# Kernel optimization log

Measured on AMD Instinct MI355X. Metric: run time of the kernel, lower is better.

The kernel has to match this reference:

```python
import jax, jax.numpy as jnp
import numpy as np

# --- QTIP TCQ config (matches init_kwargs) ---
M, K = 4096, 4096          # out_features, in_features
TD_X, TD_Y = 16, 16        # tile dims
L = 16                     # trellis state bits
KV = 4                     # bits consumed per step (K=2 bits/weight * V=2)
V = 2                      # weights emitted per step
TLUT_BITS = 9              # lut index bits
T_STEPS = TD_X * TD_Y // V # 128 steps per tile
NBITS = T_STEPS * KV       # 512 bits per tile (tail-biting: exactly K bits/weight)
NWORDS = NBITS // 16       # 32 int16 words per tile
NT = (M // TD_X) * (K // TD_Y)  # 65536 tiles
BATCH, SEQ = 4, 2048


def setup_inputs() -> dict:
    key = jax.random.key(0)
    k1, k2, k3 = jax.random.split(key, 3)
    inp = jax.random.normal(k1, (BATCH, SEQ, K), dtype=jnp.float32)
    # int16 buffer modeled as int32 holding arbitrary 16-bit patterns
    trellis = jax.random.randint(k2, (NT, NWORDS), 0, 65536, dtype=jnp.int32)
    tlut = jax.random.normal(k3, (2 ** TLUT_BITS, V), dtype=jnp.float32) * 0.02
    return {"inp": inp, "trellis": trellis, "tlut": tlut}


def _decode(trellis, tlut):
    """Decode bit-packed tail-biting bitshift trellis codes into dense W [M, K]."""
    words = trellis.astype(jnp.uint32) & 0xFFFF          # uint16 bit patterns
    shifts = (15 - jnp.arange(16)).astype(jnp.uint32)    # MSB-first within word
    bits = ((words[:, :, None] >> shifts) & 1).astype(jnp.int32).reshape(NT, NBITS)
    # step t reads L-bit window starting at t*KV, wrapping around (tail-biting)
    win = (jnp.arange(T_STEPS)[:, None] * KV + jnp.arange(L)[None, :]) % NBITS  # [T, L]
    bw = bits[:, win]                                    # [NT, T, L]
    pow2 = (2 ** (L - 1 - jnp.arange(L))).astype(jnp.int32)
    state = jnp.einsum('ntl,l->nt', bw, pow2)            # L-bit state per step
    code = state & (2 ** TLUT_BITS - 1)                  # low tlut_bits index the lut
    w = tlut[code].reshape(NT, TD_X, TD_Y)               # V outputs/step, row-major tile
    # tiles are laid out row-major over (M//td_x, K//td_y)
    w = w.reshape(M // TD_X, K // TD_Y, TD_X, TD_Y).transpose(0, 2, 1, 3).reshape(M, K)
    return w


def reference(inp, trellis, tlut):
    Wd = _decode(trellis, tlut)          # [M, K]
    x = inp.reshape(-1, K)               # [bs, K]
    y = x @ Wd.T                         # [bs, M]
    return y.reshape(*inp.shape[:-1], M).astype(inp.dtype)
```

## Files before the change

### kernel.cpp

```cpp
#include <hip/hip_runtime.h>
#include <hip/hip_bf16.h>

#define AS1 __attribute__((address_space(1)))
#define AS3 __attribute__((address_space(3)))

typedef __bf16 bf16x8 __attribute__((ext_vector_type(8)));
typedef float f32x4 __attribute__((ext_vector_type(4)));

#define GLOAD_LDS16(gptr, lptr) \
  __builtin_amdgcn_global_load_lds((AS1 void*)(gptr), (AS3 void*)(lptr), 16, 0, 0)

#define M_W   4096
#define K_DIM 4096
#define M_X   8192
#define NT_T  65536
#define NKT   (K_DIM/64)

#define BAR()        __builtin_amdgcn_s_barrier()
#define WAIT_VM4()   asm volatile("s_waitcnt vmcnt(4)" ::: "memory")
#define WAIT_VM0()   asm volatile("s_waitcnt vmcnt(0)" ::: "memory")

__device__ __forceinline__ unsigned short f2bf(float f) {
  unsigned int u = __float_as_uint(f);
  unsigned int r = (u + 0x7FFFu + ((u >> 16) & 1u)) >> 16;
  return (unsigned short)r;
}

__global__ void prep_kernel(const float* __restrict__ x,
                            const int* __restrict__ trellis,
                            const float* __restrict__ tlut,
                            unsigned short* __restrict__ xb,
                            unsigned short* __restrict__ W) {
  int b = blockIdx.x;
  int tid = threadIdx.x;
  if (b % 3 == 0) {
    int idx = (b / 3) * 256 + tid;
    const float4* p = reinterpret_cast<const float4*>(x) + (size_t)idx * 2;
    float4 u = p[0];
    float4 v = p[1];
    uint4 o;
    o.x = (unsigned)f2bf(u.x) | ((unsigned)f2bf(u.y) << 16);
    o.y = (unsigned)f2bf(u.z) | ((unsigned)f2bf(u.w) << 16);
    o.z = (unsigned)f2bf(v.x) | ((unsigned)f2bf(v.y) << 16);
    o.w = (unsigned)f2bf(v.z) | ((unsigned)f2bf(v.w) << 16);
    reinterpret_cast<uint4*>(xb)[idx] = o;
  } else {
    int db = b - b / 3 - 1;
    int idx = db * 256 + tid;
    int t = idx >> 7;
    int s = idx & 127;
    const unsigned int* tr = reinterpret_cast<const unsigned int*>(trellis) + t * 32;
    int w0  = s >> 2;
    int off = (s & 3) * 4;
    unsigned int a = tr[w0] & 0xFFFFu;
    unsigned int state;
    if (off == 0) {
      state = a;
    } else {
      unsigned int bb = tr[(w0 + 1) & 31] & 0xFFFFu;
      state = ((a << off) | (bb >> (16 - off))) & 0xFFFFu;
    }
    unsigned int code = state & 0x1FFu;
    float2 v = reinterpret_cast<const float2*>(tlut)[code];
    int i = t >> 8;
    int j = t & 255;
    int flat = s * 2;
    int r = flat >> 4;
    int c = flat & 15;
    unsigned int packed = (unsigned)f2bf(v.x) | ((unsigned)f2bf(v.y) << 16);
    size_t o = (size_t)(i * 16 + r) * K_DIM + (j * 16 + c);
    *reinterpret_cast<unsigned int*>(W + o) = packed;
  }
}


template<int BUF, int MH>
__device__ __forceinline__ void lda(const char* ldsc, const int* aRow, const int* kOff,
                                    bf16x8 (&af)[4][2]) {
  const char* base = ldsc + (BUF * 2 + MH) * 16384;
  #pragma unroll
  for (int fm = 0; fm < 4; ++fm)
    #pragma unroll
    for (int kh = 0; kh < 2; ++kh)
      af[fm][kh] = *(const bf16x8*)(base + aRow[fm] + kOff[kh]);
}

template<int BUF, int NH>
__device__ __forceinline__ void ldb(const char* ldsc, const int* bRow, const int* kOff,
                                    bf16x8 (&bq)[2][2]) {
  const char* base = ldsc + 65536 + (BUF * 2 + NH) * 16384;
  #pragma unroll
  for (int fn = 0; fn < 2; ++fn)
    #pragma unroll
    for (int kh = 0; kh < 2; ++kh)
      bq[fn][kh] = *(const bf16x8*)(base + bRow[fn] + kOff[kh]);
}

template<int MH, int NH>
__device__ __forceinline__ void mm(const bf16x8 (&af)[4][2], const bf16x8 (&bq)[2][2],
                                   f32x4 (&acc)[8][4]) {
  #pragma unroll
  for (int fm = 0; fm < 4; ++fm)
    #pragma unroll
    for (int fn = 0; fn < 2; ++fn)
      #pragma unroll
      for (int kh = 0; kh < 2; ++kh)
        acc[MH * 4 + fm][NH * 2 + fn] =
            __builtin_amdgcn_mfma_f32_16x16x32_bf16(af[fm][kh], bq[fn][kh],
                                                    acc[MH * 4 + fm][NH * 2 + fn], 0, 0, 0);
}

template<int BUF, int HALF>
__device__ __forceinline__ void stA(const unsigned short* xb, char* ldsc, int kt,
                                    int gArow0, int gArow1, int gcol, int lo0) {
  const unsigned short* s0 = xb + (size_t)(gArow0 + HALF * 64) * K_DIM + kt * 64 + gcol;
  const unsigned short* s1 = xb + (size_t)(gArow1 + HALF * 64) * K_DIM + kt * 64 + gcol;
  GLOAD_LDS16(s0, ldsc + (BUF * 2 + HALF) * 16384 + lo0);
  GLOAD_LDS16(s1, ldsc + (BUF * 2 + HALF) * 16384 + lo0 + 1024);
}

template<int BUF, int HALF>
__device__ __forceinline__ void stB(const unsigned short* W, char* ldsc, int kt,
                                    int gBrow0, int gBrow1, int gcol, int lo0) {
  const unsigned short* s0 = W + (size_t)(gBrow0 + HALF * 32) * K_DIM + kt * 64 + gcol;
  const unsigned short* s1 = W + (size_t)(gBrow1 + HALF * 32) * K_DIM + kt * 64 + gcol;
  GLOAD_LDS16(s0, ldsc + 65536 + (BUF * 2 + HALF) * 16384 + lo0);
  GLOAD_LDS16(s1, ldsc + 65536 + (BUF * 2 + HALF) * 16384 + lo0 + 1024);
}

__global__ __launch_bounds__(512) void gemm8_kernel(const unsigned short* __restrict__ xb,
                                                    const unsigned short* __restrict__ W,
                                                    float* __restrict__ y) {
  extern __shared__ __align__(16) char ldsc[];

  int bid = blockIdx.x;
  int swz = (bid & 7) * 64 + (bid >> 3);
  int brow = (swz >> 4) * 256;
  int bcol = (swz & 15) * 256;

  int tid  = threadIdx.x;
  int lane = tid & 63;
  int wid  = tid >> 6;
  int wr = wid >> 2;
  int wc = wid & 3;

  int kOff[2], aRow[4], bRow[2];
  #pragma unroll
  for (int kh = 0; kh < 2; ++kh) kOff[kh] = ((kh * 4 + (lane >> 4)) ^ (lane & 7)) << 4;
  #pragma unroll
  for (int fm = 0; fm < 4; ++fm) aRow[fm] = (wr * 64 + fm * 16 + (lane & 15)) << 7;
  #pragma unroll
  for (int fn = 0; fn < 2; ++fn) bRow[fn] = (wc * 32 + fn * 16 + (lane & 15)) << 7;

  int q0 = wid * 16 + (lane >> 3);
  int q1 = q0 + 8;
  int lo0 = wid * 2048 + lane * 16;
  int gcol = ((lane & 7) ^ (lane >> 3)) << 3;
  int gArow0 = brow + (q0 >> 6) * 128 + (q0 & 63);
  int gArow1 = brow + (q1 >> 6) * 128 + (q1 & 63);
  int gBrow0 = bcol + (q0 >> 5) * 64 + (q0 & 31);
  int gBrow1 = bcol + (q1 >> 5) * 64 + (q1 & 31);

  f32x4 acc[8][4];
  #pragma unroll
  for (int m = 0; m < 8; ++m)
    #pragma unroll
    for (int n = 0; n < 4; ++n)
      acc[m][n] = (f32x4){0.f, 0.f, 0.f, 0.f};

  bf16x8 af[4][2];
  bf16x8 bq0[2][2], bq1[2][2];

  stA<0,0>(xb, ldsc, 0, gArow0, gArow1, gcol, lo0);
  stB<0,0>(W,  ldsc, 0, gBrow0, gBrow1, gcol, lo0);
  stB<0,1>(W,  ldsc, 0, gBrow0, gBrow1, gcol, lo0);
  stA<0,1>(xb, ldsc, 0, gArow0, gArow1, gcol, lo0);
  stA<1,0>(xb, ldsc, 1, gArow0, gArow1, gcol, lo0);
  stB<1,0>(W,  ldsc, 1, gBrow0, gBrow1, gcol, lo0);
  WAIT_VM0(); BAR();

  #pragma unroll 1
  for (int i = 0; i < NKT / 2; ++i) {
    int t1 = 2 * i + 1;
    int t2 = 2 * i + 2; if (t2 > NKT - 1) t2 = NKT - 1;
    int t3 = 2 * i + 3; if (t3 > NKT - 1) t3 = NKT - 1;

    lda<0,0>(ldsc, aRow, kOff, af);
    ldb<0,0>(ldsc, bRow, kOff, bq0);
    ldb<0,1>(ldsc, bRow, kOff, bq1);
    stB<1,1>(W,  ldsc, t1, gBrow0, gBrow1, gcol, lo0);
    stA<1,1>(xb, ldsc, t1, gArow0, gArow1, gcol, lo0);
    BAR();
    __builtin_amdgcn_s_setprio(1);
    mm<0,0>(af, bq0, acc);
    mm<0,1>(af, bq1, acc);
    __builtin_amdgcn_s_setprio(0);
    WAIT_VM4(); BAR();

    lda<0,1>(ldsc, aRow, kOff, af);
    stA<0,0>(xb, ldsc, t2, gArow0, gArow1, gcol, lo0);
    stB<0,0>(W,  ldsc, t2, gBrow0, gBrow1, gcol, lo0);
    BAR();
    __builtin_amdgcn_s_setprio(1);
    mm<1,0>(af, bq0, acc);
    mm<1,1>(af, bq1, acc);
    __builtin_amdgcn_s_setprio(0);
    WAIT_VM4(); BAR();

    lda<1,0>(ldsc, aRow, kOff, af);
    ldb<1,0>(ldsc, bRow, kOff, bq0);
    ldb<1,1>(ldsc, bRow, kOff, bq1);
    stB<0,1>(W,  ldsc, t2, gBrow0, gBrow1, gcol, lo0);
    stA<0,1>(xb, ldsc, t2, gArow0, gArow1, gcol, lo0);
    BAR();
    __builtin_amdgcn_s_setprio(1);
    mm<0,0>(af, bq0, acc);
    mm<0,1>(af, bq1, acc);
    __builtin_amdgcn_s_setprio(0);
    WAIT_VM4(); BAR();

    lda<1,1>(ldsc, aRow, kOff, af);
    stA<1,0>(xb, ldsc, t3, gArow0, gArow1, gcol, lo0);
    stB<1,0>(W,  ldsc, t3, gBrow0, gBrow1, gcol, lo0);
    BAR();
    __builtin_amdgcn_s_setprio(1);
    mm<1,0>(af, bq0, acc);
    mm<1,1>(af, bq1, acc);
    __builtin_amdgcn_s_setprio(0);
    WAIT_VM4(); BAR();
  }

  WAIT_VM0(); BAR();

  #pragma unroll
  for (int am = 0; am < 8; ++am) {
    #pragma unroll
    for (int an = 0; an < 4; ++an) {
      int row0 = brow + wr * 128 + am * 16 + (lane >> 4) * 4;
      int col  = bcol + wc * 64 + an * 16 + (lane & 15);
      #pragma unroll
      for (int j = 0; j < 4; ++j)
        y[(size_t)(row0 + j) * M_W + col] = acc[am][an][j];
    }
  }
}

extern "C" void kernel_launch(void* const* d_in, const int* in_sizes, int n_in,
                              void* d_out, int out_size, void* d_ws, size_t ws_size,
                              hipStream_t stream) {
  const float* inp     = (const float*)d_in[0];
  const int*   trellis = (const int*)d_in[1];
  const float* tlut    = (const float*)d_in[2];
  float* y = (float*)d_out;

  unsigned short* xb = (unsigned short*)d_ws;
  unsigned short* Wd = (unsigned short*)((char*)d_ws + (size_t)M_X * K_DIM * 2);

  (void)hipFuncSetAttribute((const void*)gemm8_kernel,
                            hipFuncAttributeMaxDynamicSharedMemorySize, 131072);

  prep_kernel<<<49152, 256, 0, stream>>>(inp, trellis, tlut, xb, Wd);
  gemm8_kernel<<<dim3(512), dim3(512), 131072, stream>>>(xb, Wd, y);
}
```

Baseline: 267.3 us.

## Software-pipeline LDS fragment loads behind MFMA with double-buffered registers

Restructures the GEMM main loop so LDS-to-register fragment loads for the next phase are issued right after the current MFMA block, using double-buffered A/B register sets. This removes one barrier per phase and the stall where MFMAs waited on fresh LDS reads. The prologue now preloads the full second k-tile and the first fragments. In exchange it uses more VGPRs, which could lower occupancy, and it depends on the reworked barrier and wait ordering to keep LDS buffers from being overwritten too early.

```diff
diff --git a/kernel.cpp b/kernel.cpp
--- a/kernel.cpp
+++ b/kernel.cpp
@@ -96,18 +96,22 @@
       bq[fn][kh] = *(const bf16x8*)(base + bRow[fn] + kOff[kh]);
 }
 
-template<int MH, int NH>
-__device__ __forceinline__ void mm(const bf16x8 (&af)[4][2], const bf16x8 (&bq)[2][2],
-                                   f32x4 (&acc)[8][4]) {
-  #pragma unroll
-  for (int fm = 0; fm < 4; ++fm)
-    #pragma unroll
-    for (int fn = 0; fn < 2; ++fn)
+template<int MH>
+__device__ __forceinline__ void mmF(const bf16x8 (&af)[4][2], const bf16x8 (&bq)[2][2][2],
+                                    f32x4 (&acc)[8][4]) {
+  __builtin_amdgcn_s_setprio(1);
+  #pragma unroll
+  for (int NH = 0; NH < 2; ++NH)
+    #pragma unroll
+    for (int fm = 0; fm < 4; ++fm)
       #pragma unroll
-      for (int kh = 0; kh < 2; ++kh)
-        acc[MH * 4 + fm][NH * 2 + fn] =
-            __builtin_amdgcn_mfma_f32_16x16x32_bf16(af[fm][kh], bq[fn][kh],
-                                                    acc[MH * 4 + fm][NH * 2 + fn], 0, 0, 0);
+      for (int fn = 0; fn < 2; ++fn)
+        #pragma unroll
+        for (int kh = 0; kh < 2; ++kh)
+          acc[MH * 4 + fm][NH * 2 + fn] =
+              __builtin_amdgcn_mfma_f32_16x16x32_bf16(af[fm][kh], bq[NH][fn][kh],
+                                                      acc[MH * 4 + fm][NH * 2 + fn], 0, 0, 0);
+  __builtin_amdgcn_s_setprio(0);
 }
 
 template<int BUF, int HALF>
@@ -168,8 +172,8 @@
     for (int n = 0; n < 4; ++n)
       acc[m][n] = (f32x4){0.f, 0.f, 0.f, 0.f};
 
-  bf16x8 af[4][2];
-  bf16x8 bq0[2][2], bq1[2][2];
+  bf16x8 afA[4][2], afB[4][2];
+  bf16x8 bqE[2][2][2], bqO[2][2][2];
 
   stA<0,0>(xb, ldsc, 0, gArow0, gArow1, gcol, lo0);
   stB<0,0>(W,  ldsc, 0, gBrow0, gBrow1, gcol, lo0);
@@ -177,60 +181,49 @@
   stA<0,1>(xb, ldsc, 0, gArow0, gArow1, gcol, lo0);
   stA<1,0>(xb, ldsc, 1, gArow0, gArow1, gcol, lo0);
   stB<1,0>(W,  ldsc, 1, gBrow0, gBrow1, gcol, lo0);
+  stB<1,1>(W,  ldsc, 1, gBrow0, gBrow1, gcol, lo0);
+  stA<1,1>(xb, ldsc, 1, gArow0, gArow1, gcol, lo0);
   WAIT_VM0(); BAR();
+
+  lda<0,0>(ldsc, aRow, kOff, afA);
+  ldb<0,0>(ldsc, bRow, kOff, bqE[0]);
+  ldb<0,1>(ldsc, bRow, kOff, bqE[1]);
 
   #pragma unroll 1
   for (int i = 0; i < NKT / 2; ++i) {
-    int t1 = 2 * i + 1;
     int t2 = 2 * i + 2; if (t2 > NKT - 1) t2 = NKT - 1;
     int t3 = 2 * i + 3; if (t3 > NKT - 1) t3 = NKT - 1;
 
-    lda<0,0>(ldsc, aRow, kOff, af);
-    ldb<0,0>(ldsc, bRow, kOff, bq0);
-    ldb<0,1>(ldsc, bRow, kOff, bq1);
-    stB<1,1>(W,  ldsc, t1, gBrow0, gBrow1, gcol, lo0);
-    stA<1,1>(xb, ldsc, t1, gArow0, gArow1, gcol, lo0);
-    BAR();
-    __builtin_amdgcn_s_setprio(1);
-    mm<0,0>(af, bq0, acc);
-    mm<0,1>(af, bq1, acc);
-    __builtin_amdgcn_s_setprio(0);
-    WAIT_VM4(); BAR();
-
-    lda<0,1>(ldsc, aRow, kOff, af);
+    mmF<0>(afA, bqE, acc);
+    lda<0,1>(ldsc, aRow, kOff, afB);
     stA<0,0>(xb, ldsc, t2, gArow0, gArow1, gcol, lo0);
     stB<0,0>(W,  ldsc, t2, gBrow0, gBrow1, gcol, lo0);
-    BAR();
-    __builtin_amdgcn_s_setprio(1);
-    mm<1,0>(af, bq0, acc);
-    mm<1,1>(af, bq1, acc);
-    __builtin_amdgcn_s_setprio(0);
-    WAIT_VM4(); BAR();
-
-    lda<1,0>(ldsc, aRow, kOff, af);
-    ldb<1,0>(ldsc, bRow, kOff, bq0);
-    ldb<1,1>(ldsc, bRow, kOff, bq1);
+    WAIT_VM4(); BAR();
+
+    mmF<1>(afB, bqE, acc);
+    lda<1,0>(ldsc, aRow, kOff, afA);
+    ldb<1,0>(ldsc, bRow, kOff, bqO[0]);
+    ldb<1,1>(ldsc, bRow, kOff, bqO[1]);
     stB<0,1>(W,  ldsc, t2, gBrow0, gBrow1, gcol, lo0);
     stA<0,1>(xb, ldsc, t2, gArow0, gArow1, gcol, lo0);
-    BAR();
-    __builtin_amdgcn_s_setprio(1);
-    mm<0,0>(af, bq0, acc);
-    mm<0,1>(af, bq1, acc);
-    __builtin_amdgcn_s_setprio(0);
-    WAIT_VM4(); BAR();
-
-    lda<1,1>(ldsc, aRow, kOff, af);
+    WAIT_VM4(); BAR();
+
+    mmF<0>(afA, bqO, acc);
+    lda<1,1>(ldsc, aRow, kOff, afB);
     stA<1,0>(xb, ldsc, t3, gArow0, gArow1, gcol, lo0);
     stB<1,0>(W,  ldsc, t3, gBrow0, gBrow1, gcol, lo0);
-    BAR();
-    __builtin_amdgcn_s_setprio(1);
-    mm<1,0>(af, bq0, acc);
-    mm<1,1>(af, bq1, acc);
-    __builtin_amdgcn_s_setprio(0);
+    WAIT_VM4(); BAR();
+
+    mmF<1>(afB, bqO, acc);
+    lda<0,0>(ldsc, aRow, kOff, afA);
+    ldb<0,0>(ldsc, bRow, kOff, bqE[0]);
+    ldb<0,1>(ldsc, bRow, kOff, bqE[1]);
+    stB<1,1>(W,  ldsc, t3, gBrow0, gBrow1, gcol, lo0);
+    stA<1,1>(xb, ldsc, t3, gArow0, gArow1, gcol, lo0);
     WAIT_VM4(); BAR();
   }
 
-  WAIT_VM0(); BAR();
+  WAIT_VM0();
 
   #pragma unroll
   for (int am = 0; am < 8; ++am) {
```

After: 254.2 us. 1.05x faster.
